# Optimization experiments

Measured on AMD Instinct MI355X. Metric: run time of the kernel, lower is better.

The kernel has to match this reference:

```python
import jax, jax.numpy as jnp
import numpy as np

B, N, D = 2, 2048, 1024
RANK, HEADS = 256, 16
HS = RANK // HEADS          # 16, low-rank head size for QK
DH = D // HEADS             # 64, value head size
SCALE = 1.0 / np.sqrt(HS)


def setup_inputs() -> dict:
    key = jax.random.key(0)
    k1, k2, k3 = jax.random.split(key, 3)
    x = jax.random.normal(k1, (B, N, D), dtype=jnp.float32)
    # causal additive mask, 0 on/below diag, -1e9 above
    mask = jnp.where(jnp.tril(jnp.ones((N, N), dtype=bool)), 0.0, -1e9).astype(jnp.float32)
    Wqk = jax.random.normal(k2, (2 * RANK, D), dtype=jnp.float32) * (1.0 / np.sqrt(D))
    Wv = jax.random.normal(k3, (D, D), dtype=jnp.float32) * (1.0 / np.sqrt(D))
    return {"x": x, "mask": mask, "Wqk": Wqk, "Wv": Wv}


def reference(x, mask, Wqk, Wv):
    b, n, d = x.shape
    qk = jnp.einsum('bnd,rd->bnr', x, Wqk)            # [b,n,2*rank]
    q, k = jnp.split(qk, 2, axis=-1)                  # [b,n,rank] each
    # L2 normalize over FULL rank dim (before head split), clamp norm >= 1e-6
    q = q / jnp.maximum(jnp.linalg.norm(q, axis=-1, keepdims=True), 1e-6)
    k = k / jnp.maximum(jnp.linalg.norm(k, axis=-1, keepdims=True), 1e-6)
    q = q.reshape(b, n, HEADS, HS).transpose(0, 2, 1, 3)   # [b,h,n,hs]
    k = k.reshape(b, n, HEADS, HS).transpose(0, 2, 1, 3)
    v = jnp.einsum('bnd,ed->bne', x, Wv).reshape(b, n, HEADS, DH).transpose(0, 2, 1, 3)  # [b,h,n,dh]
    att = jnp.einsum('bhqe,bhke->bhqk', q, k) * SCALE
    att = jnp.clip(att, -10000.0, 10000.0)
    att = att + mask[None, None, :, :]
    att = jax.nn.softmax(att, axis=-1)
    # NaN guard: zero NaNs then renormalize (no-op when no NaNs)
    att = jnp.where(jnp.isnan(att), 0.0, att)
    att = att / jnp.maximum(att.sum(axis=-1, keepdims=True), 1e-6)
    y = jnp.einsum('bhqk,bhkd->bhqd', att, v)              # [b,h,n,dh]
    return y.transpose(0, 2, 1, 3).reshape(b, n, d)
```

## Files before the change

### kernel.cpp

```cpp
#include <hip/hip_runtime.h>
#include <math.h>

#define BATCH 2
#define SEQ   2048
#define DIM   1024
#define RANK  256
#define HEADS 16
#define HS    16
#define DH    64
#define MROWS 4096

#define QSCALE 0.36067376f

typedef __attribute__((ext_vector_type(8)))  short    short8;
typedef __attribute__((ext_vector_type(4)))  float    f32x4;
typedef __attribute__((ext_vector_type(16))) float    f32x16;
typedef __attribute__((ext_vector_type(2)))  unsigned uint2v;

#define GPTR const __attribute__((address_space(1))) unsigned int*
#define LPTR __attribute__((address_space(3))) unsigned int*

__device__ __forceinline__ unsigned short f2bf(float f) {
    union { float f; unsigned u; } v; v.f = f;
    return (unsigned short)((v.u + 0x7FFFu + ((v.u >> 16) & 1u)) >> 16);
}
__device__ __forceinline__ float bf2f(unsigned short h) {
    union { unsigned u; float f; } v; v.u = ((unsigned)h) << 16;
    return v.f;
}

#define XQ   1048576
#define WQKQ 131072
#define WVQ  262144
__global__ __launch_bounds__(256) void conv3(const float* __restrict__ x,
                                             const float* __restrict__ wqk,
                                             const float* __restrict__ wv,
                                             unsigned short* __restrict__ xb,
                                             unsigned short* __restrict__ wcat)
{
    const int i = blockIdx.x * 256 + threadIdx.x;
    const float* src; unsigned short* dst; int j;
    if (i < XQ)              { src = x;   dst = xb;   j = i; }
    else if (i < XQ + WQKQ)  { src = wqk; dst = wcat; j = i - XQ; }
    else                     { src = wv;  dst = wcat + (size_t)4 * WQKQ; j = i - XQ - WQKQ; }
    float4 v = ((const float4*)src)[j];
    ushort4 o; o.x = f2bf(v.x); o.y = f2bf(v.y); o.z = f2bf(v.z); o.w = f2bf(v.w);
    ((ushort4*)dst)[j] = o;
}

__global__ __launch_bounds__(256) void gemm_mfma(const unsigned short* __restrict__ A,
                                                 const unsigned short* __restrict__ W,
                                                 unsigned short* __restrict__ qkb,
                                                 unsigned short* __restrict__ vt)
{
    __shared__ __align__(16) unsigned short Alds[128 * 64];
    __shared__ __align__(16) unsigned short Blds[64 * 64];

    const int tid = threadIdx.x;
    const int w = tid >> 6, lane = tid & 63;
    const int lr = lane & 15, lg = lane >> 4;
    const int wm = w >> 1, wn = w & 1;

    const int Lf = blockIdx.x;
    const int wg = (Lf & 7) * 96 + (Lf >> 3);
    const int bm = (wg & 31) * 128;
    const int bn = (wg >> 5) * 64;

    const int rs = lane >> 3, cs = lane & 7;

    f32x4 acc[4][2] = {};

    for (int k0 = 0; k0 < 1024; k0 += 64) {
        __syncthreads();
        #pragma unroll
        for (int i = 0; i < 4; ++i) {
            const int r = w * 32 + i * 8 + rs;
            __builtin_amdgcn_global_load_lds(
                (GPTR)&A[(size_t)(bm + r) * 1024 + k0 + 8 * (cs ^ (r & 7))],
                (LPTR)&Alds[(w * 32 + i * 8) * 64], 16, 0, 0);
        }
        #pragma unroll
        for (int i = 0; i < 2; ++i) {
            const int r = w * 16 + i * 8 + rs;
            __builtin_amdgcn_global_load_lds(
                (GPTR)&W[(size_t)(bn + r) * 1024 + k0 + 8 * (cs ^ (r & 7))],
                (LPTR)&Blds[(w * 16 + i * 8) * 64], 16, 0, 0);
        }
        __syncthreads();

        #pragma unroll
        for (int kk = 0; kk < 2; ++kk) {
            short8 af[4], bfr[2];
            #pragma unroll
            for (int mi = 0; mi < 4; ++mi) {
                const int row = wm * 64 + mi * 16 + lr;
                af[mi] = *(const short8*)&Alds[row * 64 + 8 * ((kk * 4 + lg) ^ (row & 7))];
            }
            #pragma unroll
            for (int ni = 0; ni < 2; ++ni) {
                const int row = wn * 32 + ni * 16 + lr;
                bfr[ni] = *(const short8*)&Blds[row * 64 + 8 * ((kk * 4 + lg) ^ (row & 7))];
            }
            #pragma unroll
            for (int mi = 0; mi < 4; ++mi)
                #pragma unroll
                for (int ni = 0; ni < 2; ++ni)
                    acc[mi][ni] = __builtin_amdgcn_mfma_f32_16x16x32_bf16(af[mi], bfr[ni], acc[mi][ni], 0, 0, 0);
        }
    }

    if (bn < 512) {
        #pragma unroll
        for (int mi = 0; mi < 4; ++mi) {
            const int rbase = bm + wm * 64 + mi * 16 + lg * 4;
            #pragma unroll
            for (int ni = 0; ni < 2; ++ni) {
                const int col = bn + wn * 32 + ni * 16 + lr;
                #pragma unroll
                for (int r = 0; r < 4; ++r)
                    qkb[(size_t)(rbase + r) * 512 + col] = f2bf(acc[mi][ni][r]);
            }
        }
    } else {
        const int nb = bn - 512;
        #pragma unroll
        for (int mi = 0; mi < 4; ++mi) {
            const int m = bm + wm * 64 + mi * 16 + lg * 4;
            const int bb = m >> 11, ms = m & 2047;
            #pragma unroll
            for (int ni = 0; ni < 2; ++ni) {
                const int d = nb + wn * 32 + ni * 16 + lr;
                ushort4 pk;
                pk.x = f2bf(acc[mi][ni][0]); pk.y = f2bf(acc[mi][ni][1]);
                pk.z = f2bf(acc[mi][ni][2]); pk.w = f2bf(acc[mi][ni][3]);
                *(ushort4*)&vt[((size_t)bb * DIM + d) * SEQ + ms] = pk;
            }
        }
    }
}

__global__ __launch_bounds__(256) void l2norm_split(const unsigned short* __restrict__ qkb,
                                                    unsigned short* __restrict__ qn,
                                                    unsigned short* __restrict__ kn)
{
    const int row = blockIdx.x;
    const int t = threadIdx.x;
    const unsigned short* p = qkb + (size_t)row * 512;
    float q = bf2f(p[t]);
    float k = bf2f(p[t + 256]);
    float sq = q * q, sk = k * k;
    #pragma unroll
    for (int off = 32; off > 0; off >>= 1) {
        sq += __shfl_down(sq, off);
        sk += __shfl_down(sk, off);
    }
    __shared__ float sh[8];
    const int wid = t >> 6;
    if ((t & 63) == 0) { sh[wid * 2] = sq; sh[wid * 2 + 1] = sk; }
    __syncthreads();
    sq = sh[0] + sh[2] + sh[4] + sh[6];
    sk = sh[1] + sh[3] + sh[5] + sh[7];
    const float rq = QSCALE / fmaxf(sqrtf(sq), 1e-6f);
    const float rk = 1.0f   / fmaxf(sqrtf(sk), 1e-6f);

    const int b = row >> 11, n = row & 2047;
    const int head = t >> 4, hs = t & 15;
    const size_t o = (((size_t)b * HEADS + head) * SEQ + n) * 16 + hs;
    qn[o] = f2bf(q * rq);
    kn[o] = f2bf(k * rk);
}


template<bool MASK>
__device__ __forceinline__ void segpv(const f32x16& s0, const f32x16& s1, int kb, int hi,
                                      int qg, const short8 vb[4][2], f32x16 o[2], float& lp)
{
    float p0[16], p1[16];
    #pragma unroll
    for (int r = 0; r < 16; ++r) {
        float e0 = __builtin_exp2f(s0[r]);
        float e1 = __builtin_exp2f(s1[r]);
        if (MASK) {
            const int kl = kb + (r & 3) + 8 * (r >> 2) + 4 * hi;
            e0 = (kl > qg) ? 0.0f : e0;
            e1 = (kl + 32 > qg) ? 0.0f : e1;
        }
        p0[r] = e0; p1[r] = e1;
        lp += e0 + e1;
    }

    short8 pa[4];
    #pragma unroll
    for (int g = 0; g < 4; ++g) {
        const float* pc = (g < 2) ? p0 : p1;
        const int jj = 2 * (g & 1);
        unsigned a0, a1, b0, b1;
        asm("v_cvt_pk_bf16_f32 %0, %1, %2" : "=v"(a0) : "v"(pc[4*jj]),     "v"(pc[4*jj + 1]));
        asm("v_cvt_pk_bf16_f32 %0, %1, %2" : "=v"(b0) : "v"(pc[4*jj + 2]), "v"(pc[4*jj + 3]));
        asm("v_cvt_pk_bf16_f32 %0, %1, %2" : "=v"(a1) : "v"(pc[4*jj + 4]), "v"(pc[4*jj + 5]));
        asm("v_cvt_pk_bf16_f32 %0, %1, %2" : "=v"(b1) : "v"(pc[4*jj + 6]), "v"(pc[4*jj + 7]));
        const uint2v r0 = __builtin_amdgcn_permlane32_swap(a0, a1, false, false);
        const uint2v r1 = __builtin_amdgcn_permlane32_swap(b0, b1, false, false);
        union { short8 s; unsigned u[4]; } pu;
        pu.u[0] = r0[0]; pu.u[1] = r1[0]; pu.u[2] = r0[1]; pu.u[3] = r1[1];
        pa[g] = pu.s;
    }

    #pragma unroll
    for (int g = 0; g < 4; ++g)
        #pragma unroll
        for (int half = 0; half < 2; ++half)
            o[half] = __builtin_amdgcn_mfma_f32_32x32x16_bf16(pa[g], vb[g][half], o[half], 0, 0, 0);
}

__global__ __launch_bounds__(256, 2) void attn_v2(const unsigned short* __restrict__ qn,
                                                  const unsigned short* __restrict__ kn,
                                                  const unsigned short* __restrict__ vt,
                                                  float* __restrict__ out)
{
    const int L = blockIdx.x;
    const int bh = L & 31;
    const int p  = L >> 5;
    const int h = bh & 15, b = bh >> 4;

    const int tid = threadIdx.x, w = tid >> 6, lane = tid & 63;
    const int qh = w >> 1, kh = w & 1;
    const int l31 = lane & 31, hi = lane >> 5;

    const int qt0 = 31 - p, qt1 = p;
    const int nt0 = (qt0 >> 1) + 1;
    const int nt1 = (qt1 >> 1) + 1;
    const int qband0 = qt0 * 64 + qh * 32, qband1 = qt1 * 64 + qh * 32;
    const int qg0 = qband0 + l31, qg1 = qband1 + l31;

    __shared__ __align__(16) unsigned char smem[33792];

    const unsigned short* qbh = qn + (size_t)bh * SEQ * 16;
    const unsigned short* kbh = kn + (size_t)bh * SEQ * 16;

    const short8 bq0 = *(const short8*)&qbh[qg0 * 16 + 8 * hi];
    const short8 bq1 = *(const short8*)&qbh[qg1 * 16 + 8 * hi];

    f32x16 o0[2] = {}, o1[2] = {};
    float lp0 = 0.0f, lp1 = 0.0f;
    const f32x16 z = {};

    const unsigned short* kwin = kbh + (64 * kh + l31) * 16 + 8 * hi;
    short8 ak0 = *(const short8*)(kwin);
    short8 ak1 = *(const short8*)(kwin + 32 * 16);

    const int vsub = lane >> 4, vslot = lane & 15;

#define STAGEV(kt_, buf_) do {                                                                    \
        const int k0_ = (kt_) * 128;                                                              \
        _Pragma("unroll")                                                                         \
        for (int i = 0; i < 4; ++i) {                                                             \
            const int dh = w * 16 + i * 4 + vsub;                                                 \
            const int so = 8 * (vslot ^ (dh & 7));                                                \
            __builtin_amdgcn_global_load_lds(                                                     \
                (GPTR)&vt[((size_t)b * DIM + h * DH + dh) * SEQ + k0_ + so],                      \
                (LPTR)(smem + (buf_) * 16384 + (w * 4 + i) * 1024), 16, 0, 0);                    \
        }                                                                                         \
    } while (0)

    STAGEV(0, 0);

    #pragma unroll 1
    for (int kt = 0; kt < nt0; ++kt) {
        short8 an0 = ak0, an1 = ak1;
        if (kt + 1 < nt0) {
            STAGEV(kt + 1, (kt + 1) & 1);
            an0 = *(const short8*)(kwin + (size_t)(kt + 1) * 128 * 16);
            an1 = *(const short8*)(kwin + (size_t)(kt + 1) * 128 * 16 + 32 * 16);
            asm volatile("s_waitcnt vmcnt(6)" ::: "memory");
        } else {
            asm volatile("s_waitcnt vmcnt(0)" ::: "memory");
        }
        __builtin_amdgcn_sched_barrier(0);
        __builtin_amdgcn_s_barrier();

        const unsigned short* Vs = (const unsigned short*)(smem + (kt & 1) * 16384);
        const int kb = kt * 128 + 64 * kh;

        short8 vb[4][2];
        #pragma unroll
        for (int g = 0; g < 4; ++g)
            #pragma unroll
            for (int half = 0; half < 2; ++half) {
                const int row = half * 32 + l31;
                const int slot = (8 * kh + 2 * g + hi) ^ (row & 7);
                vb[g][half] = *(const short8*)&Vs[row * 128 + 8 * slot];
            }

        __builtin_amdgcn_s_setprio(1);
        if (kt < nt0 - 1) {
            const f32x16 s0 = __builtin_amdgcn_mfma_f32_32x32x16_bf16(ak0, bq0, z, 0, 0, 0);
            const f32x16 s1 = __builtin_amdgcn_mfma_f32_32x32x16_bf16(ak1, bq0, z, 0, 0, 0);
            segpv<false>(s0, s1, kb, hi, qg0, vb, o0, lp0);
        } else if (kb <= qband0 + 31) {
            const f32x16 s0 = __builtin_amdgcn_mfma_f32_32x32x16_bf16(ak0, bq0, z, 0, 0, 0);
            const f32x16 s1 = __builtin_amdgcn_mfma_f32_32x32x16_bf16(ak1, bq0, z, 0, 0, 0);
            if (kb + 63 <= qband0) segpv<false>(s0, s1, kb, hi, qg0, vb, o0, lp0);
            else                   segpv<true >(s0, s1, kb, hi, qg0, vb, o0, lp0);
        }
        if (kt < nt1) {
            const f32x16 s0 = __builtin_amdgcn_mfma_f32_32x32x16_bf16(ak0, bq1, z, 0, 0, 0);
            const f32x16 s1 = __builtin_amdgcn_mfma_f32_32x32x16_bf16(ak1, bq1, z, 0, 0, 0);
            if (kt < nt1 - 1) {
                segpv<false>(s0, s1, kb, hi, qg1, vb, o1, lp1);
            } else if (kb <= qband1 + 31) {
                if (kb + 63 <= qband1) segpv<false>(s0, s1, kb, hi, qg1, vb, o1, lp1);
                else                   segpv<true >(s0, s1, kb, hi, qg1, vb, o1, lp1);
            }
        }
        __builtin_amdgcn_s_setprio(0);

        ak0 = an0; ak1 = an1;
        __builtin_amdgcn_s_barrier();
    }
#undef STAGEV

    __syncthreads();
    float* Os0 = (float*)smem;
    float* Os1 = (float*)(smem + 16384);
    float* Ls0 = (float*)(smem + 32768);
    float* Ls1 = (float*)(smem + 33280);

    if (kh == 1) {
        #pragma unroll
        for (int half = 0; half < 2; ++half)
            #pragma unroll
            for (int r = 0; r < 16; ++r) {
                const int q = (r & 3) + 8 * (r >> 2) + 4 * hi;
                Os0[(qh * 32 + q) * 64 + half * 32 + l31] = o0[half][r];
                Os1[(qh * 32 + q) * 64 + half * 32 + l31] = o1[half][r];
            }
        Ls0[qh * 64 + lane] = lp0;
        Ls1[qh * 64 + lane] = lp1;
    }
    __syncthreads();
    if (kh == 0) {
        float lt0 = lp0 + Ls0[qh * 64 + lane];
        float lt1 = lp1 + Ls1[qh * 64 + lane];
        lt0 += __shfl_xor(lt0, 32);
        lt1 += __shfl_xor(lt1, 32);
        const float inv0 = 1.0f / fmaxf(lt0, 1e-6f);
        const float inv1 = 1.0f / fmaxf(lt1, 1e-6f);
        #pragma unroll
        for (int r = 0; r < 16; ++r) {
            const int q = (r & 3) + 8 * (r >> 2) + 4 * hi;
            const float iv0 = __shfl(inv0, q);
            const float iv1 = __shfl(inv1, q);
            #pragma unroll
            for (int half = 0; half < 2; ++half) {
                const float v0 = (o0[half][r] + Os0[(qh * 32 + q) * 64 + half * 32 + l31]) * iv0;
                const float v1 = (o1[half][r] + Os1[(qh * 32 + q) * 64 + half * 32 + l31]) * iv1;
                __builtin_nontemporal_store(v0,
                    &out[((size_t)b * SEQ + qband0 + q) * DIM + h * DH + half * 32 + l31]);
                __builtin_nontemporal_store(v1,
                    &out[((size_t)b * SEQ + qband1 + q) * DIM + h * DH + half * 32 + l31]);
            }
        }
    }
}

extern "C" void kernel_launch(void* const* d_in, const int* in_sizes, int n_in,
                              void* d_out, int out_size, void* d_ws, size_t ws_size,
                              hipStream_t stream)
{
    const float* x   = (const float*)d_in[0];
    const float* Wqk = (const float*)d_in[2];
    const float* Wv  = (const float*)d_in[3];
    float* out = (float*)d_out;

    unsigned short* xb   = (unsigned short*)d_ws;
    unsigned short* qkb  = xb  + (size_t)MROWS * DIM;
    unsigned short* vt   = qkb + (size_t)MROWS * 512;
    unsigned short* wcat = vt  + (size_t)BATCH * DIM * SEQ;
    unsigned short* qn = xb;
    unsigned short* kn = xb + (size_t)32 * SEQ * 16;

    conv3<<<5632, 256, 0, stream>>>(x, Wqk, Wv, xb, wcat);
    gemm_mfma<<<768, 256, 0, stream>>>(xb, wcat, qkb, vt);
    l2norm_split<<<MROWS, 256, 0, stream>>>(qkb, qn, kn);
    attn_v2<<<512, 256, 0, stream>>>(qn, kn, vt, out);
}
```

Before: 70.56 us.

## Double-buffer GEMM LDS tiles and split attention query tiles across 8 waves

The projection GEMM now double-buffers its A/B LDS tiles with async global-to-LDS prefetch of the next k-step, so loads overlap MFMA work instead of being separated by full syncs. The attention kernel moves from 256 to 512 threads, giving each of the two paired query tiles its own group of four waves instead of one wave processing both. It also streams V fragments from LDS inside segpv and interleaves the two QK MFMAs with the softmax work to cut register pressure. The cost is more LDS traffic and barrier coupling between the two tile groups, and the short-tile group idles on later iterations while it waits at barriers.

```diff
diff --git a/kernel.cpp b/kernel.cpp
--- a/kernel.cpp
+++ b/kernel.cpp
@@ -48,13 +48,13 @@
     ((ushort4*)dst)[j] = o;
 }
 
-__global__ __launch_bounds__(256) void gemm_mfma(const unsigned short* __restrict__ A,
-                                                 const unsigned short* __restrict__ W,
-                                                 unsigned short* __restrict__ qkb,
-                                                 unsigned short* __restrict__ vt)
-{
-    __shared__ __align__(16) unsigned short Alds[128 * 64];
-    __shared__ __align__(16) unsigned short Blds[64 * 64];
+__global__ __launch_bounds__(256, 3) void gemm_mfma(const unsigned short* __restrict__ A,
+                                                    const unsigned short* __restrict__ W,
+                                                    unsigned short* __restrict__ qkb,
+                                                    unsigned short* __restrict__ vt)
+{
+    __shared__ __align__(16) unsigned short Alds[2][128 * 64];
+    __shared__ __align__(16) unsigned short Blds[2][64 * 64];
 
     const int tid = threadIdx.x;
     const int w = tid >> 6, lane = tid & 63;
@@ -70,36 +70,50 @@
 
     f32x4 acc[4][2] = {};
 
-    for (int k0 = 0; k0 < 1024; k0 += 64) {
-        __syncthreads();
-        #pragma unroll
-        for (int i = 0; i < 4; ++i) {
-            const int r = w * 32 + i * 8 + rs;
-            __builtin_amdgcn_global_load_lds(
-                (GPTR)&A[(size_t)(bm + r) * 1024 + k0 + 8 * (cs ^ (r & 7))],
-                (LPTR)&Alds[(w * 32 + i * 8) * 64], 16, 0, 0);
-        }
-        #pragma unroll
-        for (int i = 0; i < 2; ++i) {
-            const int r = w * 16 + i * 8 + rs;
-            __builtin_amdgcn_global_load_lds(
-                (GPTR)&W[(size_t)(bn + r) * 1024 + k0 + 8 * (cs ^ (r & 7))],
-                (LPTR)&Blds[(w * 16 + i * 8) * 64], 16, 0, 0);
-        }
-        __syncthreads();
-
+#define STAGEG(kt_, buf_) do {                                                        \
+        const int k0_ = (kt_) * 64;                                                   \
+        _Pragma("unroll")                                                             \
+        for (int i = 0; i < 4; ++i) {                                                 \
+            const int r = w * 32 + i * 8 + rs;                                        \
+            __builtin_amdgcn_global_load_lds(                                         \
+                (GPTR)&A[(size_t)(bm + r) * 1024 + k0_ + 8 * (cs ^ (r & 7))],         \
+                (LPTR)&Alds[buf_][(w * 32 + i * 8) * 64], 16, 0, 0);                  \
+        }                                                                             \
+        _Pragma("unroll")                                                             \
+        for (int i = 0; i < 2; ++i) {                                                 \
+            const int r = w * 16 + i * 8 + rs;                                        \
+            __builtin_amdgcn_global_load_lds(                                         \
+                (GPTR)&W[(size_t)(bn + r) * 1024 + k0_ + 8 * (cs ^ (r & 7))],         \
+                (LPTR)&Blds[buf_][(w * 16 + i * 8) * 64], 16, 0, 0);                  \
+        }                                                                             \
+    } while (0)
+
+    STAGEG(0, 0);
+
+    #pragma unroll 1
+    for (int kt = 0; kt < 16; ++kt) {
+        if (kt + 1 < 16) {
+            STAGEG(kt + 1, (kt + 1) & 1);
+            asm volatile("s_waitcnt vmcnt(6)" ::: "memory");
+        } else {
+            asm volatile("s_waitcnt vmcnt(0)" ::: "memory");
+        }
+        __builtin_amdgcn_sched_barrier(0);
+        __builtin_amdgcn_s_barrier();
+
+        const int buf = kt & 1;
         #pragma unroll
         for (int kk = 0; kk < 2; ++kk) {
             short8 af[4], bfr[2];
             #pragma unroll
             for (int mi = 0; mi < 4; ++mi) {
                 const int row = wm * 64 + mi * 16 + lr;
-                af[mi] = *(const short8*)&Alds[row * 64 + 8 * ((kk * 4 + lg) ^ (row & 7))];
+                af[mi] = *(const short8*)&Alds[buf][row * 64 + 8 * ((kk * 4 + lg) ^ (row & 7))];
             }
             #pragma unroll
             for (int ni = 0; ni < 2; ++ni) {
                 const int row = wn * 32 + ni * 16 + lr;
-                bfr[ni] = *(const short8*)&Blds[row * 64 + 8 * ((kk * 4 + lg) ^ (row & 7))];
+                bfr[ni] = *(const short8*)&Blds[buf][row * 64 + 8 * ((kk * 4 + lg) ^ (row & 7))];
             }
             #pragma unroll
             for (int mi = 0; mi < 4; ++mi)
@@ -107,7 +121,9 @@
                 for (int ni = 0; ni < 2; ++ni)
                     acc[mi][ni] = __builtin_amdgcn_mfma_f32_16x16x32_bf16(af[mi], bfr[ni], acc[mi][ni], 0, 0, 0);
         }
-    }
+        __builtin_amdgcn_s_barrier();
+    }
+#undef STAGEG
 
     if (bn < 512) {
         #pragma unroll
@@ -172,48 +188,80 @@
 
 
 template<bool MASK>
-__device__ __forceinline__ void segpv(const f32x16& s0, const f32x16& s1, int kb, int hi,
-                                      int qg, const short8 vb[4][2], f32x16 o[2], float& lp)
-{
-    float p0[16], p1[16];
-    #pragma unroll
-    for (int r = 0; r < 16; ++r) {
-        float e0 = __builtin_exp2f(s0[r]);
-        float e1 = __builtin_exp2f(s1[r]);
-        if (MASK) {
-            const int kl = kb + (r & 3) + 8 * (r >> 2) + 4 * hi;
-            e0 = (kl > qg) ? 0.0f : e0;
-            e1 = (kl + 32 > qg) ? 0.0f : e1;
-        }
-        p0[r] = e0; p1[r] = e1;
-        lp += e0 + e1;
-    }
-
+__device__ __forceinline__ void segpv(const short8 ak0, const short8 ak1, const short8 bq,
+                                      const unsigned short* Vs, int kb, int kh, int hi,
+                                      int l31, int qg, f32x16 o[2], float& lp)
+{
+    const f32x16 z = {};
     short8 pa[4];
-    #pragma unroll
-    for (int g = 0; g < 4; ++g) {
-        const float* pc = (g < 2) ? p0 : p1;
-        const int jj = 2 * (g & 1);
-        unsigned a0, a1, b0, b1;
-        asm("v_cvt_pk_bf16_f32 %0, %1, %2" : "=v"(a0) : "v"(pc[4*jj]),     "v"(pc[4*jj + 1]));
-        asm("v_cvt_pk_bf16_f32 %0, %1, %2" : "=v"(b0) : "v"(pc[4*jj + 2]), "v"(pc[4*jj + 3]));
-        asm("v_cvt_pk_bf16_f32 %0, %1, %2" : "=v"(a1) : "v"(pc[4*jj + 4]), "v"(pc[4*jj + 5]));
-        asm("v_cvt_pk_bf16_f32 %0, %1, %2" : "=v"(b1) : "v"(pc[4*jj + 6]), "v"(pc[4*jj + 7]));
-        const uint2v r0 = __builtin_amdgcn_permlane32_swap(a0, a1, false, false);
-        const uint2v r1 = __builtin_amdgcn_permlane32_swap(b0, b1, false, false);
-        union { short8 s; unsigned u[4]; } pu;
-        pu.u[0] = r0[0]; pu.u[1] = r1[0]; pu.u[2] = r0[1]; pu.u[3] = r1[1];
-        pa[g] = pu.s;
+
+    const f32x16 s0 = __builtin_amdgcn_mfma_f32_32x32x16_bf16(ak0, bq, z, 0, 0, 0);
+    {
+        float p0[16];
+        #pragma unroll
+        for (int r = 0; r < 16; ++r) {
+            float e = __builtin_exp2f(s0[r]);
+            if (MASK) {
+                const int kl = kb + (r & 3) + 8 * (r >> 2) + 4 * hi;
+                e = (kl > qg) ? 0.0f : e;
+            }
+            p0[r] = e; lp += e;
+        }
+        #pragma unroll
+        for (int g = 0; g < 2; ++g) {
+            const int jj = 2 * g;
+            unsigned a0, a1, b0, b1;
+            asm("v_cvt_pk_bf16_f32 %0, %1, %2" : "=v"(a0) : "v"(p0[4*jj]),     "v"(p0[4*jj + 1]));
+            asm("v_cvt_pk_bf16_f32 %0, %1, %2" : "=v"(b0) : "v"(p0[4*jj + 2]), "v"(p0[4*jj + 3]));
+            asm("v_cvt_pk_bf16_f32 %0, %1, %2" : "=v"(a1) : "v"(p0[4*jj + 4]), "v"(p0[4*jj + 5]));
+            asm("v_cvt_pk_bf16_f32 %0, %1, %2" : "=v"(b1) : "v"(p0[4*jj + 6]), "v"(p0[4*jj + 7]));
+            const uint2v r0 = __builtin_amdgcn_permlane32_swap(a0, a1, false, false);
+            const uint2v r1 = __builtin_amdgcn_permlane32_swap(b0, b1, false, false);
+            union { short8 s; unsigned u[4]; } pu;
+            pu.u[0] = r0[0]; pu.u[1] = r1[0]; pu.u[2] = r0[1]; pu.u[3] = r1[1];
+            pa[g] = pu.s;
+        }
+    }
+    const f32x16 s1 = __builtin_amdgcn_mfma_f32_32x32x16_bf16(ak1, bq, z, 0, 0, 0);
+    {
+        float p1[16];
+        #pragma unroll
+        for (int r = 0; r < 16; ++r) {
+            float e = __builtin_exp2f(s1[r]);
+            if (MASK) {
+                const int kl = kb + 32 + (r & 3) + 8 * (r >> 2) + 4 * hi;
+                e = (kl > qg) ? 0.0f : e;
+            }
+            p1[r] = e; lp += e;
+        }
+        #pragma unroll
+        for (int g = 0; g < 2; ++g) {
+            const int jj = 2 * g;
+            unsigned a0, a1, b0, b1;
+            asm("v_cvt_pk_bf16_f32 %0, %1, %2" : "=v"(a0) : "v"(p1[4*jj]),     "v"(p1[4*jj + 1]));
+            asm("v_cvt_pk_bf16_f32 %0, %1, %2" : "=v"(b0) : "v"(p1[4*jj + 2]), "v"(p1[4*jj + 3]));
+            asm("v_cvt_pk_bf16_f32 %0, %1, %2" : "=v"(a1) : "v"(p1[4*jj + 4]), "v"(p1[4*jj + 5]));
+            asm("v_cvt_pk_bf16_f32 %0, %1, %2" : "=v"(b1) : "v"(p1[4*jj + 6]), "v"(p1[4*jj + 7]));
+            const uint2v r0 = __builtin_amdgcn_permlane32_swap(a0, a1, false, false);
+            const uint2v r1 = __builtin_amdgcn_permlane32_swap(b0, b1, false, false);
+            union { short8 s; unsigned u[4]; } pu;
+            pu.u[0] = r0[0]; pu.u[1] = r1[0]; pu.u[2] = r0[1]; pu.u[3] = r1[1];
+            pa[2 + g] = pu.s;
+        }
     }
 
     #pragma unroll
     for (int g = 0; g < 4; ++g)
         #pragma unroll
-        for (int half = 0; half < 2; ++half)
-            o[half] = __builtin_amdgcn_mfma_f32_32x32x16_bf16(pa[g], vb[g][half], o[half], 0, 0, 0);
-}
-
-__global__ __launch_bounds__(256, 2) void attn_v2(const unsigned short* __restrict__ qn,
+        for (int half = 0; half < 2; ++half) {
+            const int row = half * 32 + l31;
+            const int slot = (8 * kh + 2 * g + hi) ^ (row & 15);
+            const short8 bv = *(const short8*)&Vs[row * 128 + 8 * slot];
+            o[half] = __builtin_amdgcn_mfma_f32_32x32x16_bf16(pa[g], bv, o[half], 0, 0, 0);
+        }
+}
+
+__global__ __launch_bounds__(512, 4) void attn_w8(const unsigned short* __restrict__ qn,
                                                   const unsigned short* __restrict__ kn,
                                                   const unsigned short* __restrict__ vt,
                                                   float* __restrict__ out)
@@ -224,26 +272,24 @@
     const int h = bh & 15, b = bh >> 4;
 
     const int tid = threadIdx.x, w = tid >> 6, lane = tid & 63;
-    const int qh = w >> 1, kh = w & 1;
+    const int seg = w >> 2, qh = (w >> 1) & 1, kh = w & 1;
     const int l31 = lane & 31, hi = lane >> 5;
 
-    const int qt0 = 31 - p, qt1 = p;
-    const int nt0 = (qt0 >> 1) + 1;
-    const int nt1 = (qt1 >> 1) + 1;
-    const int qband0 = qt0 * 64 + qh * 32, qband1 = qt1 * 64 + qh * 32;
-    const int qg0 = qband0 + l31, qg1 = qband1 + l31;
+    const int qt  = seg ? p : 31 - p;
+    const int nts = (qt >> 1) + 1;
+    const int nt0 = ((31 - p) >> 1) + 1;
+    const int band = qt * 64 + qh * 32;
+    const int qg = band + l31;
 
     __shared__ __align__(16) unsigned char smem[33792];
 
     const unsigned short* qbh = qn + (size_t)bh * SEQ * 16;
     const unsigned short* kbh = kn + (size_t)bh * SEQ * 16;
 
-    const short8 bq0 = *(const short8*)&qbh[qg0 * 16 + 8 * hi];
-    const short8 bq1 = *(const short8*)&qbh[qg1 * 16 + 8 * hi];
-
-    f32x16 o0[2] = {}, o1[2] = {};
-    float lp0 = 0.0f, lp1 = 0.0f;
-    const f32x16 z = {};
+    const short8 bq = *(const short8*)&qbh[qg * 16 + 8 * hi];
+
+    f32x16 o[2] = {};
+    float lp = 0.0f;
 
     const unsigned short* kwin = kbh + (64 * kh + l31) * 16 + 8 * hi;
     short8 ak0 = *(const short8*)(kwin);
@@ -254,12 +300,13 @@
 #define STAGEV(kt_, buf_) do {                                                                    \
         const int k0_ = (kt_) * 128;                                                              \
         _Pragma("unroll")                                                                         \
-        for (int i = 0; i < 4; ++i) {                                                             \
-            const int dh = w * 16 + i * 4 + vsub;                                                 \
-            const int so = 8 * (vslot ^ (dh & 7));                                                \
+        for (int i = 0; i < 2; ++i) {                                                             \
+            const int c = 2 * w + i;                                                              \
+            const int dh = 4 * c + vsub;                                                          \
+            const int so = 8 * (vslot ^ (dh & 15));                                               \
             __builtin_amdgcn_global_load_lds(                                                     \
                 (GPTR)&vt[((size_t)b * DIM + h * DH + dh) * SEQ + k0_ + so],                      \
-                (LPTR)(smem + (buf_) * 16384 + (w * 4 + i) * 1024), 16, 0, 0);                    \
+                (LPTR)(smem + (buf_) * 16384 + c * 1024), 16, 0, 0);                              \
         }                                                                                         \
     } while (0)
 
@@ -272,59 +319,36 @@
             STAGEV(kt + 1, (kt + 1) & 1);
             an0 = *(const short8*)(kwin + (size_t)(kt + 1) * 128 * 16);
             an1 = *(const short8*)(kwin + (size_t)(kt + 1) * 128 * 16 + 32 * 16);
-            asm volatile("s_waitcnt vmcnt(6)" ::: "memory");
+            asm volatile("s_waitcnt vmcnt(4)" ::: "memory");
         } else {
             asm volatile("s_waitcnt vmcnt(0)" ::: "memory");
         }
         __builtin_amdgcn_sched_barrier(0);
         __builtin_amdgcn_s_barrier();
 
-        const unsigned short* Vs = (const unsigned short*)(smem + (kt & 1) * 16384);
-        const int kb = kt * 128 + 64 * kh;
-
-        short8 vb[4][2];
-        #pragma unroll
-        for (int g = 0; g < 4; ++g)
-            #pragma unroll
-            for (int half = 0; half < 2; ++half) {
-                const int row = half * 32 + l31;
-                const int slot = (8 * kh + 2 * g + hi) ^ (row & 7);
-                vb[g][half] = *(const short8*)&Vs[row * 128 + 8 * slot];
-            }
-
-        __builtin_amdgcn_s_setprio(1);
-        if (kt < nt0 - 1) {
-            const f32x16 s0 = __builtin_amdgcn_mfma_f32_32x32x16_bf16(ak0, bq0, z, 0, 0, 0);
-            const f32x16 s1 = __builtin_amdgcn_mfma_f32_32x32x16_bf16(ak1, bq0, z, 0, 0, 0);
-            segpv<false>(s0, s1, kb, hi, qg0, vb, o0, lp0);
-        } else if (kb <= qband0 + 31) {
-            const f32x16 s0 = __builtin_amdgcn_mfma_f32_32x32x16_bf16(ak0, bq0, z, 0, 0, 0);
-            const f32x16 s1 = __builtin_amdgcn_mfma_f32_32x32x16_bf16(ak1, bq0, z, 0, 0, 0);
-            if (kb + 63 <= qband0) segpv<false>(s0, s1, kb, hi, qg0, vb, o0, lp0);
-            else                   segpv<true >(s0, s1, kb, hi, qg0, vb, o0, lp0);
-        }
-        if (kt < nt1) {
-            const f32x16 s0 = __builtin_amdgcn_mfma_f32_32x32x16_bf16(ak0, bq1, z, 0, 0, 0);
-            const f32x16 s1 = __builtin_amdgcn_mfma_f32_32x32x16_bf16(ak1, bq1, z, 0, 0, 0);
-            if (kt < nt1 - 1) {
-                segpv<false>(s0, s1, kb, hi, qg1, vb, o1, lp1);
-            } else if (kb <= qband1 + 31) {
-                if (kb + 63 <= qband1) segpv<false>(s0, s1, kb, hi, qg1, vb, o1, lp1);
-                else                   segpv<true >(s0, s1, kb, hi, qg1, vb, o1, lp1);
-            }
-        }
-        __builtin_amdgcn_s_setprio(0);
+        if (kt < nts) {
+            const unsigned short* Vs = (const unsigned short*)(smem + (kt & 1) * 16384);
+            const int kb = kt * 128 + 64 * kh;
+            __builtin_amdgcn_s_setprio(1);
+            if (kt < nts - 1) {
+                segpv<false>(ak0, ak1, bq, Vs, kb, kh, hi, l31, qg, o, lp);
+            } else if (kb <= band + 31) {
+                if (kb + 63 <= band) segpv<false>(ak0, ak1, bq, Vs, kb, kh, hi, l31, qg, o, lp);
+                else                 segpv<true >(ak0, ak1, bq, Vs, kb, kh, hi, l31, qg, o, lp);
+            }
+            __builtin_amdgcn_s_setprio(0);
+        }
 
         ak0 = an0; ak1 = an1;
         __builtin_amdgcn_s_barrier();
     }
 #undef STAGEV
 
+    lp += __shfl_xor(lp, 32);
+
     __syncthreads();
-    float* Os0 = (float*)smem;
-    float* Os1 = (float*)(smem + 16384);
-    float* Ls0 = (float*)(smem + 32768);
-    float* Ls1 = (float*)(smem + 33280);
+    float* Os = (float*)(smem + seg * 16384);
+    float* Ls = (float*)(smem + 32768 + seg * 512);
 
     if (kh == 1) {
         #pragma unroll
@@ -332,33 +356,23 @@
             #pragma unroll
             for (int r = 0; r < 16; ++r) {
                 const int q = (r & 3) + 8 * (r >> 2) + 4 * hi;
-                Os0[(qh * 32 + q) * 64 + half * 32 + l31] = o0[half][r];
-                Os1[(qh * 32 + q) * 64 + half * 32 + l31] = o1[half][r];
-            }
-        Ls0[qh * 64 + lane] = lp0;
-        Ls1[qh * 64 + lane] = lp1;
+                Os[(qh * 32 + q) * 64 + half * 32 + l31] = o[half][r];
+            }
+        Ls[qh * 64 + lane] = lp;
     }
     __syncthreads();
     if (kh == 0) {
-        float lt0 = lp0 + Ls0[qh * 64 + lane];
-        float lt1 = lp1 + Ls1[qh * 64 + lane];
-        lt0 += __shfl_xor(lt0, 32);
-        lt1 += __shfl_xor(lt1, 32);
-        const float inv0 = 1.0f / fmaxf(lt0, 1e-6f);
-        const float inv1 = 1.0f / fmaxf(lt1, 1e-6f);
+        const float lt = lp + Ls[qh * 64 + lane];
+        const float inv = 1.0f / fmaxf(lt, 1e-6f);
         #pragma unroll
         for (int r = 0; r < 16; ++r) {
             const int q = (r & 3) + 8 * (r >> 2) + 4 * hi;
-            const float iv0 = __shfl(inv0, q);
-            const float iv1 = __shfl(inv1, q);
+            const float iv = __shfl(inv, q);
             #pragma unroll
             for (int half = 0; half < 2; ++half) {
-                const float v0 = (o0[half][r] + Os0[(qh * 32 + q) * 64 + half * 32 + l31]) * iv0;
-                const float v1 = (o1[half][r] + Os1[(qh * 32 + q) * 64 + half * 32 + l31]) * iv1;
-                __builtin_nontemporal_store(v0,
-                    &out[((size_t)b * SEQ + qband0 + q) * DIM + h * DH + half * 32 + l31]);
-                __builtin_nontemporal_store(v1,
-                    &out[((size_t)b * SEQ + qband1 + q) * DIM + h * DH + half * 32 + l31]);
+                const float v = (o[half][r] + Os[(qh * 32 + q) * 64 + half * 32 + l31]) * iv;
+                __builtin_nontemporal_store(v,
+                    &out[((size_t)b * SEQ + band + q) * DIM + h * DH + half * 32 + l31]);
             }
         }
     }
@@ -383,5 +397,5 @@
     conv3<<<5632, 256, 0, stream>>>(x, Wqk, Wv, xb, wcat);
     gemm_mfma<<<768, 256, 0, stream>>>(xb, wcat, qkb, vt);
     l2norm_split<<<MROWS, 256, 0, stream>>>(qkb, qn, kn);
-    attn_v2<<<512, 256, 0, stream>>>(qn, kn, vt, out);
-}
+    attn_w8<<<512, 512, 0, stream>>>(qn, kn, vt, out);
+}
```

Result: faster. 68.74 us (-2.6%).
